# Kernel tuning notes

Measured on AMD Instinct MI355X. Metric: run time of the kernel, lower is better.

The kernel has to match this reference:

```python
import jax, jax.numpy as jnp
import numpy as np

ALPHA = 0.9        # synaptic decay (hidden layers; layer 0 uses 0*syn + h)
BETA = 0.85        # membrane leak
THRESHOLD = 1.0
SIM_TIME = 50
SCALE = 100.0      # SurrGradSpike.scale


@jax.custom_vjp
def spike_fn(x):
    # Heaviside step: 1.0 where x > 0 (strict, matching torch `input > 0`)
    return (x > 0).astype(x.dtype)

def _spike_fwd(x):
    return spike_fn(x), x

def _spike_bwd(x, g):
    # normalized fast-sigmoid surrogate gradient (Zenke & Ganguli 2018)
    return (g / (SCALE * jnp.abs(x) + 1.0) ** 2,)

spike_fn.defvjp(_spike_fwd, _spike_bwd)


def setup_inputs() -> dict:
    key = jax.random.key(0)
    k0, k1, k2, k3 = jax.random.split(key, 4)
    return {
        "inputs": jax.random.normal(k0, (128, 1024), dtype=jnp.float32),
        "W0": jax.random.normal(k1, (1024, 2048), dtype=jnp.float32),
        "W1": jax.random.normal(k2, (2048, 2048), dtype=jnp.float32),
        "W2": jax.random.normal(k3, (2048, 512), dtype=jnp.float32),
    }


def _dsnn_forward(inputs, weights):
    batch = inputs.shape[0]
    n_layers = len(weights)
    syn0 = tuple(jnp.zeros((batch, W.shape[1]), dtype=inputs.dtype) for W in weights)
    mem0 = tuple(jnp.zeros((batch, W.shape[1]), dtype=inputs.dtype) for W in weights)

    def step(carry, _):
        syn, mem = carry
        new_syn, new_mem = [], []
        prev_spk = None
        for l, W in enumerate(weights):
            # feedforward drive: static input at layer 0, current-step spikes after
            h = inputs @ W if l == 0 else prev_spk @ W
            # layer 0: new_syn = 0*syn + h ; others: alpha*syn + h
            s = h if l == 0 else ALPHA * syn[l] + h
            m = BETA * mem[l] + s
            mthr = m - THRESHOLD
            out = spike_fn(mthr)
            if l < n_layers - 1:
                # hard reset to 0 where spiked (output layer never resets)
                m = jnp.where(mthr > 0, jnp.zeros_like(m), m)
            prev_spk = out
            new_syn.append(s)
            new_mem.append(m)
        return (tuple(new_syn), tuple(new_mem)), None

    (syn, mem), _ = jax.lax.scan(step, (syn0, mem0), None, length=SIM_TIME)
    # torch returns mem_rec[-1][-1]: output-layer membrane at final timestep
    return mem[-1]


def reference(inputs, W0, W1, W2):
    return _dsnn_forward(inputs, (W0, W1, W2))
```

## Files before the change

kernel.cpp:

```cpp
#include <hip/hip_runtime.h>
#include <hip/hip_bf16.h>

#define ALPHA 0.9f
#define BETA  0.85f
#define TSIM  50
#define BATCH 128
#define N0    1024
#define N1    2048
#define N2    2048
#define N3    512

#define A50   0.00515379f
#define B50   0.000295764f
#define INVAB 20.0f

typedef __attribute__((ext_vector_type(8))) short bf16x8;
typedef __attribute__((ext_vector_type(8))) unsigned short ushort8;
typedef __attribute__((ext_vector_type(4))) float f32x4;

#define GLOBAL_AS __attribute__((address_space(1)))
#define LDS_AS    __attribute__((address_space(3)))

#define R32(X) X(0) X(1) X(2) X(3) X(4) X(5) X(6) X(7) X(8) X(9) X(10) X(11) \
               X(12) X(13) X(14) X(15) X(16) X(17) X(18) X(19) X(20) X(21)   \
               X(22) X(23) X(24) X(25) X(26) X(27) X(28) X(29) X(30) X(31)
#define R18(X) X(32) X(33) X(34) X(35) X(36) X(37) X(38) X(39) X(40) X(41)   \
               X(42) X(43) X(44) X(45) X(46) X(47) X(48) X(49)
#define R50(X) R32(X) R18(X)

#define DECLC(t)   float c##t = 0.f;
#define PROBELO(t) c##t += w * (float)((lo >> (t)) & 1u);
#define PROBEHI(t) c##t += w * (float)((hi >> ((t) - 32)) & 1u);
#define STEPT(t)                                                  \
    s = ALPHA * s + (base + c##t);                                \
    m = BETA * m + s;                                             \
    if (m - 1.f > 0.f) { a2 += (pa - pb) * INVAB; m = 0.f; }      \
    pa *= inva;                                                   \
    pb *= invb;

__global__ __launch_bounds__(256) void gemm_f32_splitk(const float* __restrict__ A,
                                                       const float* __restrict__ B,
                                                       float* __restrict__ Cp,
                                                       int M, int N, int K, int KC) {
    __shared__ float As[16][65];
    __shared__ float Bs[16][68];

    const int tid = threadIdx.x;
    const int tx  = tid % 16;
    const int ty  = tid / 16;
    const int bx  = blockIdx.x;
    const int by  = blockIdx.y;
    const int z   = blockIdx.z;

    float acc[4][4] = {};

    const int ar = tid / 4;
    const int ak = (tid % 4) * 4;
    const int br = tid / 16;
    const int bc = (tid % 16) * 4;

    const int kbeg = z * KC;
    for (int k0 = kbeg; k0 < kbeg + KC; k0 += 16) {
        float4 av = *(const float4*)&A[(size_t)(by * 64 + ar) * K + k0 + ak];
        As[ak + 0][ar] = av.x;
        As[ak + 1][ar] = av.y;
        As[ak + 2][ar] = av.z;
        As[ak + 3][ar] = av.w;
        float4 bv = *(const float4*)&B[(size_t)(k0 + br) * N + bx * 64 + bc];
        *(float4*)&Bs[br][bc] = bv;
        __syncthreads();

#pragma unroll
        for (int kk = 0; kk < 16; ++kk) {
            float a0 = As[kk][ty * 4 + 0];
            float a1 = As[kk][ty * 4 + 1];
            float a2 = As[kk][ty * 4 + 2];
            float a3 = As[kk][ty * 4 + 3];
            float b0 = Bs[kk][tx * 4 + 0];
            float b1 = Bs[kk][tx * 4 + 1];
            float b2 = Bs[kk][tx * 4 + 2];
            float b3 = Bs[kk][tx * 4 + 3];
            acc[0][0] += a0 * b0; acc[0][1] += a0 * b1; acc[0][2] += a0 * b2; acc[0][3] += a0 * b3;
            acc[1][0] += a1 * b0; acc[1][1] += a1 * b1; acc[1][2] += a1 * b2; acc[1][3] += a1 * b3;
            acc[2][0] += a2 * b0; acc[2][1] += a2 * b1; acc[2][2] += a2 * b2; acc[2][3] += a2 * b3;
            acc[3][0] += a3 * b0; acc[3][1] += a3 * b1; acc[3][2] += a3 * b2; acc[3][3] += a3 * b3;
        }
        __syncthreads();
    }

#pragma unroll
    for (int i = 0; i < 4; ++i) {
        float4 v = make_float4(acc[i][0], acc[i][1], acc[i][2], acc[i][3]);
        *(float4*)&Cp[((size_t)z * M + by * 64 + ty * 4 + i) * N + bx * 64 + tx * 4] = v;
    }
}

__global__ __launch_bounds__(256) void split_transpose_fast(const float* __restrict__ W,
                                                            __hip_bfloat16* __restrict__ Th,
                                                            __hip_bfloat16* __restrict__ Tl) {
    __shared__ float Wf[128][33];

    const int tid = threadIdx.x;
    const int n0  = blockIdx.x * 32;
    const int k0  = blockIdx.y * 128;

#pragma unroll
    for (int it = 0; it < 16; ++it) {
        const int idx = it * 256 + tid;
        const int kk  = idx >> 5;
        const int nn  = idx & 31;
        Wf[kk][nn] = W[(size_t)(k0 + kk) * N2 + n0 + nn];
    }
    __syncthreads();

    const int nl  = tid >> 3;
    const int oct = tid & 7;

#pragma unroll
    for (int half = 0; half < 2; ++half) {
        const int kb = half * 64 + oct * 8;
        ushort8 vh, vl;
#pragma unroll
        for (int u = 0; u < 8; ++u) {
            const float w = Wf[kb + u][nl];
            const __hip_bfloat16 hi = __float2bfloat16(w);
            const float lo = w - __bfloat162float(hi);
            const __hip_bfloat16 lb = __float2bfloat16(lo);
            vh[u] = *(const unsigned short*)&hi;
            vl[u] = *(const unsigned short*)&lb;
        }
        const size_t o = (size_t)(n0 + nl) * N1 + k0 + kb;
        *(ushort8*)&Th[o] = vh;
        *(ushort8*)&Tl[o] = vl;
    }
}

template <int BN, int WGM, int WGN, int WMT, int WNT>
__global__ __launch_bounds__(256) void gemm_bf16_split_k(const __hip_bfloat16* __restrict__ A,
                                                         const __hip_bfloat16* __restrict__ Bh,
                                                         const __hip_bfloat16* __restrict__ Bl,
                                                         float* __restrict__ Cp,
                                                         int M, int N, int K, int KC) {
    constexpr int BM = 128;
    constexpr int BK = 32;
    constexpr int NA = (BM * BK) / (256 * 8);
    constexpr int NB = (BN * BK) / (256 * 8);

    __shared__ alignas(16) __hip_bfloat16 As[BM * BK];
    __shared__ alignas(16) __hip_bfloat16 Bhs[BN * BK];
    __shared__ alignas(16) __hip_bfloat16 Bls[BN * BK];

    const int tid  = threadIdx.x;
    const int wave = tid >> 6;
    const int lane = tid & 63;
    const int quad = lane >> 4;
    const int l16  = lane & 15;

    const int m0 = blockIdx.y * BM;
    const int n0 = blockIdx.x * BN;
    const int z  = blockIdx.z;

    const int wm = (wave % WGM) * (WMT * 16);
    const int wn = (wave / WGM) * (WNT * 16);

    f32x4 acc[WMT][WNT] = {};

    const __hip_bfloat16* agp[NA];
    int aoff[NA];
#pragma unroll
    for (int i = 0; i < NA; ++i) {
        const int c = i * 256 + tid;
        agp[i]  = A + (size_t)(m0 + (c >> 2)) * K + (c & 3) * 8;
        aoff[i] = c * 8;
    }
    const __hip_bfloat16 *bhgp[NB], *blgp[NB];
    int boff[NB];
#pragma unroll
    for (int i = 0; i < NB; ++i) {
        const int c = i * 256 + tid;
        bhgp[i] = Bh + (size_t)(n0 + (c >> 2)) * K + (c & 3) * 8;
        blgp[i] = Bl + (size_t)(n0 + (c >> 2)) * K + (c & 3) * 8;
        boff[i] = c * 8;
    }

    const int kbeg = z * KC;
    for (int k0 = kbeg; k0 < kbeg + KC; k0 += BK) {
#pragma unroll
        for (int i = 0; i < NA; ++i)
            __builtin_amdgcn_global_load_lds((const GLOBAL_AS void*)(agp[i] + k0),
                                             (LDS_AS void*)&As[aoff[i]], 16, 0, 0);
#pragma unroll
        for (int i = 0; i < NB; ++i) {
            __builtin_amdgcn_global_load_lds((const GLOBAL_AS void*)(bhgp[i] + k0),
                                             (LDS_AS void*)&Bhs[boff[i]], 16, 0, 0);
            __builtin_amdgcn_global_load_lds((const GLOBAL_AS void*)(blgp[i] + k0),
                                             (LDS_AS void*)&Bls[boff[i]], 16, 0, 0);
        }
        __syncthreads();

        bf16x8 af[WMT], bhf[WNT], blf[WNT];
#pragma unroll
        for (int i = 0; i < WMT; ++i)
            af[i] = *(const bf16x8*)&As[(wm + i * 16 + l16) * BK + quad * 8];
#pragma unroll
        for (int j = 0; j < WNT; ++j) {
            bhf[j] = *(const bf16x8*)&Bhs[(wn + j * 16 + l16) * BK + quad * 8];
            blf[j] = *(const bf16x8*)&Bls[(wn + j * 16 + l16) * BK + quad * 8];
        }
#pragma unroll
        for (int i = 0; i < WMT; ++i)
#pragma unroll
            for (int j = 0; j < WNT; ++j) {
                acc[i][j] = __builtin_amdgcn_mfma_f32_16x16x32_bf16(af[i], bhf[j], acc[i][j], 0, 0, 0);
                acc[i][j] = __builtin_amdgcn_mfma_f32_16x16x32_bf16(af[i], blf[j], acc[i][j], 0, 0, 0);
            }
        __syncthreads();
    }

#pragma unroll
    for (int i = 0; i < WMT; ++i)
#pragma unroll
        for (int j = 0; j < WNT; ++j)
#pragma unroll
            for (int r = 0; r < 4; ++r)
                Cp[((size_t)z * M + m0 + wm + i * 16 + quad * 4 + r) * N + n0 + wn + j * 16 + l16] =
                    acc[i][j][r];
}

__global__ __launch_bounds__(256) void scan_l0_classify(const float* __restrict__ P0,
                                                        __hip_bfloat16* __restrict__ C0,
                                                        int* __restrict__ jlist0,
                                                        unsigned long long* __restrict__ mask0,
                                                        int* __restrict__ count0) {
    const int b     = blockIdx.x;
    const int chunk = blockIdx.y;
    const int tid   = threadIdx.x;
    const int j     = chunk * 256 + tid;
    const int lane  = tid & 63;
    const int wv    = tid >> 6;

    float h = 0.f;
#pragma unroll
    for (int z = 0; z < 8; ++z) h += P0[((size_t)z * BATCH + b) * N1 + j];

    float m = 0.f;
    unsigned long long mask = 0ull;
#pragma unroll
    for (int t = 0; t < TSIM; ++t) {
        m = BETA * m + h;
        if (m - 1.f > 0.f) { mask |= (1ull << t); m = 0.f; }
    }
    const unsigned long long FULL = (1ull << TSIM) - 1ull;
    C0[(size_t)b * N1 + j] = __float2bfloat16((mask == FULL) ? 1.f : 0.f);

    const bool has = (mask != 0ull) && (mask != FULL);
    const unsigned long long bal = __ballot(has);

    __shared__ int wcnt[4];
    if (lane == 0) wcnt[wv] = __popcll(bal);
    __syncthreads();
    int base = 0;
#pragma unroll
    for (int w = 0; w < 4; ++w)
        if (w < wv) base += wcnt[w];
    const int pos = base + __popcll(bal & ((1ull << lane) - 1ull));

    const size_t lbase = (size_t)(b * 8 + chunk) * 256;
    if (has) {
        jlist0[lbase + pos] = j;
        mask0[lbase + pos]  = mask;
    }
    if (tid == 0) count0[b * 8 + chunk] = wcnt[0] + wcnt[1] + wcnt[2] + wcnt[3];
}

__global__ __launch_bounds__(256, 2) void h1_scan_a2(const float* __restrict__ PB1,
                                                     const float* __restrict__ W1,
                                                     const int* __restrict__ jlist0,
                                                     const unsigned long long* __restrict__ mask0,
                                                     const int* __restrict__ count0,
                                                     float* __restrict__ A2) {
    const int b  = blockIdx.x;
    const int jc = blockIdx.y * 256 + threadIdx.x;

    float base = 0.f;
#pragma unroll
    for (int z = 0; z < 16; ++z) base += PB1[((size_t)z * BATCH + b) * N2 + jc];

    R50(DECLC)

    for (int c = 0; c < 8; ++c) {
        const int cnt      = count0[b * 8 + c];
        const size_t lbase = (size_t)(b * 8 + c) * 256;
        for (int e = 0; e < cnt; ++e) {
            const unsigned long long mk = mask0[lbase + e];
            const int j                 = jlist0[lbase + e];
            const float w               = W1[(size_t)j * N2 + jc];
            const unsigned lo = (unsigned)mk, hi = (unsigned)(mk >> 32);
            R32(PROBELO)
            R18(PROBEHI)
        }
    }

    float s = 0.f, m = 0.f, a2 = 0.f;
    float pa = A50, pb = B50;
    const float inva = 1.0f / ALPHA, invb = 1.0f / BETA;
    R50(STEPT)

    A2[(size_t)b * N2 + jc] = a2;
}

__global__ __launch_bounds__(256) void reduce_out(const float* __restrict__ PB2,
                                                  float* __restrict__ out) {
    const int idx = blockIdx.x * 256 + threadIdx.x;
    float v = 0.f;
#pragma unroll
    for (int z = 0; z < 16; ++z) v += PB2[(size_t)z * (BATCH * N3) + idx];
    out[idx] = v;
}

extern "C" void kernel_launch(void* const* d_in, const int* in_sizes, int n_in,
                              void* d_out, int out_size, void* d_ws, size_t ws_size,
                              hipStream_t stream) {
    const float* inputs = (const float*)d_in[0];
    const float* W0     = (const float*)d_in[1];
    const float* W1     = (const float*)d_in[2];
    const float* W2     = (const float*)d_in[3];
    float* out = (float*)d_out;

    float* P0  = (float*)d_ws;
    float* PB1 = P0 + 8 * BATCH * N1;
    float* A2  = PB1 + 16 * BATCH * N2;
    float* PB2 = A2 + BATCH * N2;
    unsigned long long* mk0 = (unsigned long long*)(PB2 + 16 * BATCH * N3);
    __hip_bfloat16* C0bf = (__hip_bfloat16*)(mk0 + BATCH * 8 * 256);
    __hip_bfloat16* W1th = C0bf + (size_t)BATCH * N1;
    __hip_bfloat16* W1tl = W1th + (size_t)N2 * N1;
    int* jl0  = (int*)(W1tl + (size_t)N2 * N1);
    int* cnt0 = jl0 + BATCH * 8 * 256;

    split_transpose_fast<<<dim3(N2 / 32, N1 / 128), 256, 0, stream>>>(W1, W1th, W1tl);

    gemm_f32_splitk<<<dim3(N1 / 64, BATCH / 64, 8), 256, 0, stream>>>(
        inputs, W0, P0, BATCH, N1, N0, N0 / 8);

    scan_l0_classify<<<dim3(BATCH, N1 / 256), 256, 0, stream>>>(P0, C0bf, jl0, mk0, cnt0);

    gemm_bf16_split_k<128, 2, 2, 4, 4>
        <<<dim3(N2 / 128, BATCH / 128, 16), 256, 0, stream>>>(
            C0bf, W1th, W1tl, PB1, BATCH, N2, N1, N1 / 16);

    h1_scan_a2<<<dim3(BATCH, N2 / 256), 256, 0, stream>>>(
        PB1, W1, jl0, mk0, cnt0, A2);

    gemm_f32_splitk<<<dim3(N3 / 64, BATCH / 64, 16), 256, 0, stream>>>(
        A2, W2, PB2, BATCH, N3, N2, N2 / 16);

    reduce_out<<<(BATCH * N3) / 256, 256, 0, stream>>>(PB2, out);
}
```

Before: 149.0 us.

## Fuse front-end stages into a cooperative persistent kernel with grid syncs

```diff
diff --git a/kernel.cpp b/kernel.cpp
--- a/kernel.cpp
+++ b/kernel.cpp
@@ -1,5 +1,8 @@
 #include <hip/hip_runtime.h>
 #include <hip/hip_bf16.h>
+#include <hip/hip_cooperative_groups.h>
+
+namespace cg = cooperative_groups;
 
 #define ALPHA 0.9f
 #define BETA  0.85f
@@ -38,19 +41,15 @@
     pa *= inva;                                                   \
     pb *= invb;
 
-__global__ __launch_bounds__(256) void gemm_f32_splitk(const float* __restrict__ A,
-                                                       const float* __restrict__ B,
-                                                       float* __restrict__ Cp,
-                                                       int M, int N, int K, int KC) {
-    __shared__ float As[16][65];
-    __shared__ float Bs[16][68];
-
+__device__ __forceinline__ void gemm_f32_core(const float* __restrict__ A,
+                                              const float* __restrict__ B,
+                                              float* __restrict__ Cp,
+                                              int M, int N, int K, int KC,
+                                              int bx, int by, int z,
+                                              float As[16][65], float Bs[16][68]) {
     const int tid = threadIdx.x;
     const int tx  = tid % 16;
     const int ty  = tid / 16;
-    const int bx  = blockIdx.x;
-    const int by  = blockIdx.y;
-    const int z   = blockIdx.z;
 
     float acc[4][4] = {};
 
@@ -95,15 +94,20 @@
     }
 }
 
-__global__ __launch_bounds__(256) void split_transpose_fast(const float* __restrict__ W,
-                                                            __hip_bfloat16* __restrict__ Th,
-                                                            __hip_bfloat16* __restrict__ Tl) {
-    __shared__ float Wf[128][33];
-
+__global__ __launch_bounds__(256) void gemm_f32_splitk(const float* __restrict__ A,
+                                                       const float* __restrict__ B,
+                                                       float* __restrict__ Cp,
+                                                       int M, int N, int K, int KC) {
+    __shared__ float As[16][65];
+    __shared__ float Bs[16][68];
+    gemm_f32_core(A, B, Cp, M, N, K, KC, blockIdx.x, blockIdx.y, blockIdx.z, As, Bs);
+}
+
+__device__ __forceinline__ void transpose_tile(const float* __restrict__ W,
+                                               __hip_bfloat16* __restrict__ Th,
+                                               __hip_bfloat16* __restrict__ Tl,
+                                               int n0, int k0, float Wf[128][33]) {
     const int tid = threadIdx.x;
-    const int n0  = blockIdx.x * 32;
-    const int k0  = blockIdx.y * 128;
-
 #pragma unroll
     for (int it = 0; it < 16; ++it) {
         const int idx = it * 256 + tid;
@@ -115,7 +119,6 @@
 
     const int nl  = tid >> 3;
     const int oct = tid & 7;
-
 #pragma unroll
     for (int half = 0; half < 2; ++half) {
         const int kb = half * 64 + oct * 8;
@@ -135,20 +138,77 @@
     }
 }
 
-template <int BN, int WGM, int WGN, int WMT, int WNT>
-__global__ __launch_bounds__(256) void gemm_bf16_split_k(const __hip_bfloat16* __restrict__ A,
-                                                         const __hip_bfloat16* __restrict__ Bh,
-                                                         const __hip_bfloat16* __restrict__ Bl,
-                                                         float* __restrict__ Cp,
-                                                         int M, int N, int K, int KC) {
-    constexpr int BM = 128;
-    constexpr int BK = 32;
-    constexpr int NA = (BM * BK) / (256 * 8);
-    constexpr int NB = (BN * BK) / (256 * 8);
-
-    __shared__ alignas(16) __hip_bfloat16 As[BM * BK];
-    __shared__ alignas(16) __hip_bfloat16 Bhs[BN * BK];
-    __shared__ alignas(16) __hip_bfloat16 Bls[BN * BK];
+__global__ __launch_bounds__(256) void split_transpose_fast(const float* __restrict__ W,
+                                                            __hip_bfloat16* __restrict__ Th,
+                                                            __hip_bfloat16* __restrict__ Tl) {
+    __shared__ float Wf[128][33];
+    transpose_tile(W, Th, Tl, blockIdx.x * 32, blockIdx.y * 128, Wf);
+}
+
+__device__ __forceinline__ void scan_l0_work(const float* __restrict__ P0,
+                                             __hip_bfloat16* __restrict__ C0,
+                                             int* __restrict__ jlist0,
+                                             unsigned long long* __restrict__ mask0,
+                                             int* __restrict__ count0,
+                                             int b, int chunk, int* wcnt) {
+    const int tid  = threadIdx.x;
+    const int j    = chunk * 256 + tid;
+    const int lane = tid & 63;
+    const int wv   = tid >> 6;
+
+    float h = 0.f;
+#pragma unroll
+    for (int z = 0; z < 8; ++z) h += P0[((size_t)z * BATCH + b) * N1 + j];
+
+    float m = 0.f;
+    unsigned long long mask = 0ull;
+#pragma unroll
+    for (int t = 0; t < TSIM; ++t) {
+        m = BETA * m + h;
+        if (m - 1.f > 0.f) { mask |= (1ull << t); m = 0.f; }
+    }
+    const unsigned long long FULL = (1ull << TSIM) - 1ull;
+    C0[(size_t)b * N1 + j] = __float2bfloat16((mask == FULL) ? 1.f : 0.f);
+
+    const bool has = (mask != 0ull) && (mask != FULL);
+    const unsigned long long bal = __ballot(has);
+
+    if (lane == 0) wcnt[wv] = __popcll(bal);
+    __syncthreads();
+    int base = 0;
+#pragma unroll
+    for (int w = 0; w < 4; ++w)
+        if (w < wv) base += wcnt[w];
+    const int pos = base + __popcll(bal & ((1ull << lane) - 1ull));
+
+    const size_t lbase = (size_t)(b * 8 + chunk) * 256;
+    if (has) {
+        jlist0[lbase + pos] = j;
+        mask0[lbase + pos]  = mask;
+    }
+    if (tid == 0) count0[b * 8 + chunk] = wcnt[0] + wcnt[1] + wcnt[2] + wcnt[3];
+    __syncthreads();
+}
+
+__global__ __launch_bounds__(256) void scan_l0_classify(const float* __restrict__ P0,
+                                                        __hip_bfloat16* __restrict__ C0,
+                                                        int* __restrict__ jlist0,
+                                                        unsigned long long* __restrict__ mask0,
+                                                        int* __restrict__ count0) {
+    __shared__ int wcnt[4];
+    scan_l0_work(P0, C0, jlist0, mask0, count0, blockIdx.x, blockIdx.y, wcnt);
+}
+
+__device__ __forceinline__ void gemm_mfma_bn64(const __hip_bfloat16* __restrict__ A,
+                                               const __hip_bfloat16* __restrict__ Bh,
+                                               const __hip_bfloat16* __restrict__ Bl,
+                                               float* __restrict__ Cp,
+                                               int bx, int z, int KC,
+                                               __hip_bfloat16* As,
+                                               __hip_bfloat16* Bhs,
+                                               __hip_bfloat16* Bls) {
+    constexpr int BM = 128, BN = 64, BK = 32;
+    const int M = BATCH, N = N2, K = N1;
 
     const int tid  = threadIdx.x;
     const int wave = tid >> 6;
@@ -156,61 +216,48 @@
     const int quad = lane >> 4;
     const int l16  = lane & 15;
 
-    const int m0 = blockIdx.y * BM;
-    const int n0 = blockIdx.x * BN;
-    const int z  = blockIdx.z;
-
-    const int wm = (wave % WGM) * (WMT * 16);
-    const int wn = (wave / WGM) * (WNT * 16);
-
-    f32x4 acc[WMT][WNT] = {};
-
-    const __hip_bfloat16* agp[NA];
-    int aoff[NA];
-#pragma unroll
-    for (int i = 0; i < NA; ++i) {
+    const int n0 = bx * BN;
+    const int wm = wave * 32;
+
+    f32x4 acc[2][4] = {};
+
+    const __hip_bfloat16* agp[2];
+    int aoff[2];
+#pragma unroll
+    for (int i = 0; i < 2; ++i) {
         const int c = i * 256 + tid;
-        agp[i]  = A + (size_t)(m0 + (c >> 2)) * K + (c & 3) * 8;
+        agp[i]  = A + (size_t)(c >> 2) * K + (c & 3) * 8;
         aoff[i] = c * 8;
     }
-    const __hip_bfloat16 *bhgp[NB], *blgp[NB];
-    int boff[NB];
-#pragma unroll
-    for (int i = 0; i < NB; ++i) {
-        const int c = i * 256 + tid;
-        bhgp[i] = Bh + (size_t)(n0 + (c >> 2)) * K + (c & 3) * 8;
-        blgp[i] = Bl + (size_t)(n0 + (c >> 2)) * K + (c & 3) * 8;
-        boff[i] = c * 8;
-    }
+    const __hip_bfloat16* bhgp = Bh + (size_t)(n0 + (tid >> 2)) * K + (tid & 3) * 8;
+    const __hip_bfloat16* blgp = Bl + (size_t)(n0 + (tid >> 2)) * K + (tid & 3) * 8;
+    const int boff = tid * 8;
 
     const int kbeg = z * KC;
     for (int k0 = kbeg; k0 < kbeg + KC; k0 += BK) {
 #pragma unroll
-        for (int i = 0; i < NA; ++i)
+        for (int i = 0; i < 2; ++i)
             __builtin_amdgcn_global_load_lds((const GLOBAL_AS void*)(agp[i] + k0),
                                              (LDS_AS void*)&As[aoff[i]], 16, 0, 0);
-#pragma unroll
-        for (int i = 0; i < NB; ++i) {
-            __builtin_amdgcn_global_load_lds((const GLOBAL_AS void*)(bhgp[i] + k0),
-                                             (LDS_AS void*)&Bhs[boff[i]], 16, 0, 0);
-            __builtin_amdgcn_global_load_lds((const GLOBAL_AS void*)(blgp[i] + k0),
-                                             (LDS_AS void*)&Bls[boff[i]], 16, 0, 0);
+        __builtin_amdgcn_global_load_lds((const GLOBAL_AS void*)(bhgp + k0),
+                                         (LDS_AS void*)&Bhs[boff], 16, 0, 0);
+        __builtin_amdgcn_global_load_lds((const GLOBAL_AS void*)(blgp + k0),
+                                         (LDS_AS void*)&Bls[boff], 16, 0, 0);
+        __syncthreads();
+
+        bf16x8 af[2], bhf[4], blf[4];
+#pragma unroll
+        for (int i = 0; i < 2; ++i)
+            af[i] = *(const bf16x8*)&As[(wm + i * 16 + l16) * BK + quad * 8];
+#pragma unroll
+        for (int j = 0; j < 4; ++j) {
+            bhf[j] = *(const bf16x8*)&Bhs[(j * 16 + l16) * BK + quad * 8];
+            blf[j] = *(const bf16x8*)&Bls[(j * 16 + l16) * BK + quad * 8];
         }
-        __syncthreads();
-
-        bf16x8 af[WMT], bhf[WNT], blf[WNT];
-#pragma unroll
-        for (int i = 0; i < WMT; ++i)
-            af[i] = *(const bf16x8*)&As[(wm + i * 16 + l16) * BK + quad * 8];
-#pragma unroll
-        for (int j = 0; j < WNT; ++j) {
-            bhf[j] = *(const bf16x8*)&Bhs[(wn + j * 16 + l16) * BK + quad * 8];
-            blf[j] = *(const bf16x8*)&Bls[(wn + j * 16 + l16) * BK + quad * 8];
-        }
-#pragma unroll
-        for (int i = 0; i < WMT; ++i)
-#pragma unroll
-            for (int j = 0; j < WNT; ++j) {
+#pragma unroll
+        for (int i = 0; i < 2; ++i)
+#pragma unroll
+            for (int j = 0; j < 4; ++j) {
                 acc[i][j] = __builtin_amdgcn_mfma_f32_16x16x32_bf16(af[i], bhf[j], acc[i][j], 0, 0, 0);
                 acc[i][j] = __builtin_amdgcn_mfma_f32_16x16x32_bf16(af[i], blf[j], acc[i][j], 0, 0, 0);
             }
@@ -218,59 +265,57 @@
     }
 
 #pragma unroll
-    for (int i = 0; i < WMT; ++i)
-#pragma unroll
-        for (int j = 0; j < WNT; ++j)
+    for (int i = 0; i < 2; ++i)
+#pragma unroll
+        for (int j = 0; j < 4; ++j)
 #pragma unroll
             for (int r = 0; r < 4; ++r)
-                Cp[((size_t)z * M + m0 + wm + i * 16 + quad * 4 + r) * N + n0 + wn + j * 16 + l16] =
+                Cp[((size_t)z * M + wm + i * 16 + quad * 4 + r) * N + n0 + j * 16 + l16] =
                     acc[i][j][r];
 }
 
-__global__ __launch_bounds__(256) void scan_l0_classify(const float* __restrict__ P0,
-                                                        __hip_bfloat16* __restrict__ C0,
-                                                        int* __restrict__ jlist0,
-                                                        unsigned long long* __restrict__ mask0,
-                                                        int* __restrict__ count0) {
-    const int b     = blockIdx.x;
-    const int chunk = blockIdx.y;
-    const int tid   = threadIdx.x;
-    const int j     = chunk * 256 + tid;
-    const int lane  = tid & 63;
-    const int wv    = tid >> 6;
-
-    float h = 0.f;
-#pragma unroll
-    for (int z = 0; z < 8; ++z) h += P0[((size_t)z * BATCH + b) * N1 + j];
-
-    float m = 0.f;
-    unsigned long long mask = 0ull;
-#pragma unroll
-    for (int t = 0; t < TSIM; ++t) {
-        m = BETA * m + h;
-        if (m - 1.f > 0.f) { mask |= (1ull << t); m = 0.f; }
-    }
-    const unsigned long long FULL = (1ull << TSIM) - 1ull;
-    C0[(size_t)b * N1 + j] = __float2bfloat16((mask == FULL) ? 1.f : 0.f);
-
-    const bool has = (mask != 0ull) && (mask != FULL);
-    const unsigned long long bal = __ballot(has);
-
-    __shared__ int wcnt[4];
-    if (lane == 0) wcnt[wv] = __popcll(bal);
+__global__ __launch_bounds__(256) void gemm3_bn64(const __hip_bfloat16* __restrict__ A,
+                                                  const __hip_bfloat16* __restrict__ Bh,
+                                                  const __hip_bfloat16* __restrict__ Bl,
+                                                  float* __restrict__ Cp, int KC) {
+    __shared__ alignas(16) __hip_bfloat16 As[128 * 32];
+    __shared__ alignas(16) __hip_bfloat16 Bhs[64 * 32];
+    __shared__ alignas(16) __hip_bfloat16 Bls[64 * 32];
+    gemm_mfma_bn64(A, Bh, Bl, Cp, blockIdx.x, blockIdx.y, KC, As, Bhs, Bls);
+}
+
+__global__ __launch_bounds__(256, 4) void mega_front(const float* __restrict__ W1,
+                                                     __hip_bfloat16* __restrict__ Th,
+                                                     __hip_bfloat16* __restrict__ Tl,
+                                                     const float* __restrict__ inputs,
+                                                     const float* __restrict__ W0,
+                                                     float* __restrict__ P0,
+                                                     __hip_bfloat16* __restrict__ C0,
+                                                     int* __restrict__ jlist0,
+                                                     unsigned long long* __restrict__ mask0,
+                                                     int* __restrict__ count0,
+                                                     float* __restrict__ PB1) {
+    __shared__ __align__(16) char smem[16896];
+    cg::grid_group grid = cg::this_grid();
+    const int bid = blockIdx.x;
+
+    transpose_tile(W1, Th, Tl, (bid & 63) * 32, (bid >> 6) * 128, (float(*)[33])smem);
     __syncthreads();
-    int base = 0;
-#pragma unroll
-    for (int w = 0; w < 4; ++w)
-        if (w < wv) base += wcnt[w];
-    const int pos = base + __popcll(bal & ((1ull << lane) - 1ull));
-
-    const size_t lbase = (size_t)(b * 8 + chunk) * 256;
-    if (has) {
-        jlist0[lbase + pos] = j;
-        mask0[lbase + pos]  = mask;
-    }
-    if (tid == 0) count0[b * 8 + chunk] = wcnt[0] + wcnt[1] + wcnt[2] + wcnt[3];
+
+    if (bid < 512)
+        gemm_f32_core(inputs, W0, P0, BATCH, N1, N0, N0 / 8,
+                      bid & 31, (bid >> 5) & 1, bid >> 6,
+                      (float(*)[65])smem, (float(*)[68])(smem + 4160));
+    grid.sync();
+
+    scan_l0_work(P0, C0, jlist0, mask0, count0, bid >> 3, bid & 7, (int*)smem);
+    grid.sync();
+
+    if (bid < 512) {
+        __hip_bfloat16* mAs = (__hip_bfloat16*)smem;
+        gemm_mfma_bn64(C0, Th, Tl, PB1, bid & 31, bid >> 5, N1 / 16,
+                       mAs, mAs + 4096, mAs + 6144);
+    }
 }
 
 __global__ __launch_bounds__(256, 2) void h1_scan_a2(const float* __restrict__ PB1,
@@ -338,16 +383,25 @@
     int* jl0  = (int*)(W1tl + (size_t)N2 * N1);
     int* cnt0 = jl0 + BATCH * 8 * 256;
 
-    split_transpose_fast<<<dim3(N2 / 32, N1 / 128), 256, 0, stream>>>(W1, W1th, W1tl);
-
-    gemm_f32_splitk<<<dim3(N1 / 64, BATCH / 64, 8), 256, 0, stream>>>(
-        inputs, W0, P0, BATCH, N1, N0, N0 / 8);
-
-    scan_l0_classify<<<dim3(BATCH, N1 / 256), 256, 0, stream>>>(P0, C0bf, jl0, mk0, cnt0);
-
-    gemm_bf16_split_k<128, 2, 2, 4, 4>
-        <<<dim3(N2 / 128, BATCH / 128, 16), 256, 0, stream>>>(
-            C0bf, W1th, W1tl, PB1, BATCH, N2, N1, N1 / 16);
+    bool coop_ok = false;
+    int maxb = 0;
+    if (hipOccupancyMaxActiveBlocksPerMultiprocessor(&maxb, (const void*)mega_front,
+                                                     256, 0) == hipSuccess &&
+        maxb >= 4) {
+        void* kargs[] = {(void*)&W1, (void*)&W1th, (void*)&W1tl, (void*)&inputs,
+                         (void*)&W0, (void*)&P0, (void*)&C0bf, (void*)&jl0,
+                         (void*)&mk0, (void*)&cnt0, (void*)&PB1};
+        if (hipLaunchCooperativeKernel((const void*)mega_front, dim3(1024), dim3(256),
+                                       kargs, 0, stream) == hipSuccess)
+            coop_ok = true;
+    }
+    if (!coop_ok) {
+        split_transpose_fast<<<dim3(N2 / 32, N1 / 128), 256, 0, stream>>>(W1, W1th, W1tl);
+        gemm_f32_splitk<<<dim3(N1 / 64, BATCH / 64, 8), 256, 0, stream>>>(
+            inputs, W0, P0, BATCH, N1, N0, N0 / 8);
+        scan_l0_classify<<<dim3(BATCH, N1 / 256), 256, 0, stream>>>(P0, C0bf, jl0, mk0, cnt0);
+        gemm3_bn64<<<dim3(N2 / 64, 16), 256, 0, stream>>>(C0bf, W1th, W1tl, PB1, N1 / 16);
+    }
 
     h1_scan_a2<<<dim3(BATCH, N2 / 256), 256, 0, stream>>>(
         PB1, W1, jl0, mk0, cnt0, A2);
```

Result: no change. 147.0 us (-1.4%).
